# Kernel optimization log

Measured on AMD Instinct MI355X. Metric: run time of the kernel, lower is better.

Reference implementation:

```python
import jax, jax.numpy as jnp
import numpy as np


def setup_inputs() -> dict:
    key = jax.random.key(0)
    ks = jax.random.split(key, 7)
    B, S, D_IN, D_K, D_V = 4, 4096, 1024, 64, 64
    s = 1.0 / np.sqrt(D_IN)
    return {
        "query": jax.random.normal(ks[0], (B, S, D_IN), jnp.float32),
        "key": jax.random.normal(ks[1], (B, S, D_IN), jnp.float32),
        "value": jax.random.normal(ks[2], (B, S, D_IN), jnp.float32),
        "Wq": jax.random.normal(ks[3], (D_IN, D_K), jnp.float32) * s,
        "bq": jnp.zeros((D_K,), jnp.float32),
        "Wk": jax.random.normal(ks[4], (D_IN, D_K), jnp.float32) * s,
        "bk": jnp.zeros((D_K,), jnp.float32),
        "Wv": jax.random.normal(ks[5], (D_IN, D_V), jnp.float32) * s,
        "bv": jnp.zeros((D_V,), jnp.float32),
    }


def reference(query, key, value, Wq, bq, Wk, bk, Wv, bv):
    # q(query) is computed twice in the original but is identical; compute once.
    q = query @ Wq + bq            # [B,S,dk]
    k = key @ Wk + bk              # [B,S,dk]
    v = value @ Wv + bv            # [B,S,dv]
    scale = jnp.asarray(q.shape[-1] ** 0.5, q.dtype)
    scores = jnp.einsum("bqd,bkd->bqk", q, k) / scale  # [B,S,S]
    probs = jax.nn.softmax(scores, axis=-1)
    return jnp.einsum("bqk,bkd->bqd", probs, v)        # [B,S,dv]
```

## Files before the change

### kernel.cpp

```cpp
#include <hip/hip_runtime.h>
#include <cmath>

constexpr int B_  = 4;
constexpr int S_  = 4096;
constexpr int DIN = 1024;
constexpr int DH  = 64;

typedef short bf16x8 __attribute__((ext_vector_type(8)));
typedef float f32x4  __attribute__((ext_vector_type(4)));

#define GPTR(p) (const __attribute__((address_space(1))) unsigned int*)(p)
#define LPTR(p) (__attribute__((address_space(3))) unsigned int*)(p)

__device__ __forceinline__ ushort f2bf(float x) {
    unsigned int u = __float_as_uint(x);
    return (ushort)((u + 0x7FFFu + ((u >> 16) & 1u)) >> 16);
}

__device__ __forceinline__ bf16x8 cvt8(f32x4 a, f32x4 b) {
    union { bf16x8 v; ushort u[8]; } r;
    r.u[0] = f2bf(a[0]); r.u[1] = f2bf(a[1]); r.u[2] = f2bf(a[2]); r.u[3] = f2bf(a[3]);
    r.u[4] = f2bf(b[0]); r.u[5] = f2bf(b[1]); r.u[6] = f2bf(b[2]); r.u[7] = f2bf(b[3]);
    return r.v;
}

#define QSCALE 0.18033688011112042f

__global__ __launch_bounds__(256) void setup_w(
    const float* __restrict__ Wq, const float* __restrict__ Wk,
    const float* __restrict__ Wv, ushort* __restrict__ Wt_g)
{
    const int y = blockIdx.y;
    const float* W = (y == 0) ? Wq : (y == 1) ? Wk : Wv;
    const int g    = blockIdx.x * 256 + threadIdx.x;
    const int lane = g & 63;
    const int nt   = (g >> 6) & 3;
    const int ks   = (g >> 8) & 1;
    const int it   = g >> 9;
    const int m    = lane & 15;
    const int quad = lane >> 4;
    const int n    = nt * 16 + m;
    const int k0   = it * 64 + (ks * 4 + quad) * 8;
    union { uint4 q; ushort u[8]; } r;
    #pragma unroll
    for (int i = 0; i < 8; ++i) r.u[i] = f2bf(W[(size_t)(k0 + i) * DH + n]);
    *(uint4*)(Wt_g + ((size_t)y << 16) + (size_t)g * 8) = r.q;
}

__global__ __launch_bounds__(256, 4) void proj_kernel(
    const float* __restrict__ Xq, const float* __restrict__ Xk, const float* __restrict__ Xv,
    const float* __restrict__ bq, const float* __restrict__ bk, const float* __restrict__ bv,
    const ushort* __restrict__ Wt_g,
    ushort* __restrict__ Qb, ushort* __restrict__ Kb, ushort* __restrict__ Vt)
{
    __shared__ __align__(16) ushort xlds[16384];

    const int y = blockIdx.y;
    const float *X, *bias;
    if (y == 0)      { X = Xq; bias = bq; }
    else if (y == 1) { X = Xk; bias = bk; }
    else             { X = Xv; bias = bv; }

    const int tid  = threadIdx.x;
    const int w    = tid >> 6;
    const int lane = tid & 63;
    const int m    = lane & 15;
    const int quad = lane >> 4;
    const int row0 = blockIdx.x * 16;

    {
        f32x4 va[8], vb[8];
        #pragma unroll
        for (int r = 0; r < 4; ++r) {
            const float* src = X + (size_t)(row0 + w * 4 + r) * DIN + lane * 8;
            #pragma unroll
            for (int sg = 0; sg < 2; ++sg) {
                va[r * 2 + sg] = *(const f32x4*)(src + sg * 512);
                vb[r * 2 + sg] = *(const f32x4*)(src + sg * 512 + 4);
            }
        }
        __builtin_amdgcn_sched_barrier(0);
        #pragma unroll
        for (int r = 0; r < 4; ++r) {
            const int row = w * 4 + r;
            #pragma unroll
            for (int sg = 0; sg < 2; ++sg) {
                const int wi = sg * 8 + (lane >> 3);
                const int fx = (lane & 7) ^ (row & 7);
                *(bf16x8*)&xlds[((wi * 16 + row) * 8 + fx) * 8] =
                    cvt8(va[r * 2 + sg], vb[r * 2 + sg]);
            }
        }
    }
    __syncthreads();

    const float bias_v = bias[w * 16 + m];
    const ushort* wbase = Wt_g + ((size_t)y << 16) + (size_t)(w * 64 + lane) * 8;

    f32x4 acc = {};
    bf16x8 wf0 = *(const bf16x8*)(wbase);
    bf16x8 wf1 = *(const bf16x8*)(wbase + 2048);
    #pragma unroll
    for (int wi = 0; wi < 16; ++wi) {
        bf16x8 nf0 = wf0, nf1 = wf1;
        if (wi < 15) {
            nf0 = *(const bf16x8*)(wbase + (size_t)(wi + 1) * 4096);
            nf1 = *(const bf16x8*)(wbase + (size_t)(wi + 1) * 4096 + 2048);
        }
        const bf16x8 a0 = *(const bf16x8*)&xlds[((wi * 16 + m) * 8 + ( quad      ^ (m & 7))) * 8];
        const bf16x8 a1 = *(const bf16x8*)&xlds[((wi * 16 + m) * 8 + ((4 + quad) ^ (m & 7))) * 8];
        acc = __builtin_amdgcn_mfma_f32_16x16x32_bf16(a0, wf0, acc, 0, 0, 0);
        acc = __builtin_amdgcn_mfma_f32_16x16x32_bf16(a1, wf1, acc, 0, 0, 0);
        wf0 = nf0; wf1 = nf1;
    }

    if (y < 2) {
        ushort* Out = (y == 0) ? Qb : Kb;
        const float sc = (y == 0) ? QSCALE : 1.0f;
        #pragma unroll
        for (int j = 0; j < 4; ++j) {
            const int row = row0 + quad * 4 + j;
            Out[(size_t)row * DH + w * 16 + m] = f2bf((acc[j] + bias_v) * sc);
        }
    } else {
        __syncthreads();
        ushort (*Vx)[32] = (ushort(*)[32])xlds;
        #pragma unroll
        for (int j = 0; j < 4; ++j)
            Vx[w * 16 + m][quad * 4 + j] = f2bf(acc[j] + bias_v);
        __syncthreads();
        const int batch = row0 >> 12;
        const int s0    = row0 & 4095;
        if (tid < 128) {
            const int d = tid >> 1, h = tid & 1;
            const uint4 v = *(const uint4*)&Vx[d][h * 8];
            *(uint4*)(Vt + ((size_t)batch * 64 + d) * S_ + s0 + h * 8) = v;
        }
    }
}

__global__ __launch_bounds__(512, 4) void attn_kernel(
    const ushort* __restrict__ Qb, const ushort* __restrict__ Kb,
    const ushort* __restrict__ Vt, float* __restrict__ Opart, float* __restrict__ Lpart)
{
    __shared__ ushort Ks[2][4096];
    __shared__ ushort Vs[2][4096];
    __shared__ ushort Pt[128 * 72];

    const int tid  = threadIdx.x;
    const int w    = tid >> 6;
    const int lane = tid & 63;
    const int m    = lane & 15;
    const int quad = lane >> 4;

    const int u  = blockIdx.x;
    const int c  = (u & 7) * 2 + ((u >> 3) >> 5);
    const int qt = (u >> 3) & 31;
    const int b  = c >> 2, jc = c & 3;
    const int q0 = qt * 128;

    bf16x8 qf[2];
    #pragma unroll
    for (int ks = 0; ks < 2; ++ks)
        qf[ks] = *(const bf16x8*)(Qb + (size_t)(b * S_ + q0 + w * 16 + m) * 64
                                     + ks * 32 + quad * 8);
    asm volatile("s_waitcnt vmcnt(0)" ::: "memory");
    __builtin_amdgcn_sched_barrier(0);

    f32x4 acc_o[4] = {};
    float Lp[4] = {};

    const ushort* kbase = Kb + (size_t)b * S_ * 64;
    const ushort* vbase = Vt + (size_t)b * 64 * S_;

    auto stage = [&](int jt, int buf) {
        const int slot = w * 64 + lane;
        const int j = slot >> 3, cc = slot & 7;
        __builtin_amdgcn_global_load_lds(
            GPTR(kbase + (size_t)(jt * 64 + j) * 64 + ((cc ^ (j & 7)) * 8)),
            LPTR(&Ks[buf][slot * 8]), 16, 0, 0);
        __builtin_amdgcn_global_load_lds(
            GPTR(vbase + (size_t)j * S_ + jt * 64 + ((cc ^ (j & 7)) * 8)),
            LPTR(&Vs[buf][slot * 8]), 16, 0, 0);
    };

    stage(jc * 16 + 0, 0);
    stage(jc * 16 + 1, 1);

    for (int it = 0; it < 16; ++it) {
        if (it < 15) asm volatile("s_waitcnt vmcnt(2)" ::: "memory");
        else         asm volatile("s_waitcnt vmcnt(0)" ::: "memory");
        __builtin_amdgcn_sched_barrier(0);
        __builtin_amdgcn_s_barrier();
        __builtin_amdgcn_sched_barrier(0);

        const ushort* ksb = Ks[it & 1];
        const ushort* vsb = Vs[it & 1];

        f32x4 acc_s[4] = {};
        #pragma unroll
        for (int ks = 0; ks < 2; ++ks)
            #pragma unroll
            for (int jt4 = 0; jt4 < 4; ++jt4) {
                const int j = jt4 * 16 + m;
                const bf16x8 kf = *(const bf16x8*)&ksb[j * 64 + (((ks * 4 + quad) ^ (j & 7)) * 8)];
                acc_s[jt4] = __builtin_amdgcn_mfma_f32_16x16x32_bf16(
                    qf[ks], kf, acc_s[jt4], 0, 0, 0);
            }

        #pragma unroll
        for (int jt4 = 0; jt4 < 4; ++jt4)
            #pragma unroll
            for (int r = 0; r < 4; ++r) {
                const float e = exp2f(acc_s[jt4][r]);
                Lp[r] += e;
                Pt[(w * 16 + quad * 4 + r) * 72 + jt4 * 16 + m] = f2bf(e);
            }

        #pragma unroll
        for (int jc2 = 0; jc2 < 2; ++jc2) {
            const bf16x8 pf = *(const bf16x8*)&Pt[(w * 16 + m) * 72 + jc2 * 32 + quad * 8];
            #pragma unroll
            for (int dt = 0; dt < 4; ++dt) {
                const int d = dt * 16 + m;
                const bf16x8 vf = *(const bf16x8*)&vsb[d * 64 + (((jc2 * 4 + quad) ^ (d & 7)) * 8)];
                acc_o[dt] = __builtin_amdgcn_mfma_f32_16x16x32_bf16(pf, vf, acc_o[dt], 0, 0, 0);
            }
        }

        __builtin_amdgcn_sched_barrier(0);
        __builtin_amdgcn_s_barrier();
        __builtin_amdgcn_sched_barrier(0);
        if (it + 2 < 16) stage(jc * 16 + it + 2, it & 1);
    }

    #pragma unroll
    for (int r = 0; r < 4; ++r) {
        float s = Lp[r];
        #pragma unroll
        for (int off = 1; off < 16; off <<= 1)
            s += __shfl_xor(s, off, 64);
        Lp[r] = s;
    }

    const size_t bj = (size_t)(b * 4 + jc);
    float* Ob = Opart + (bj << 18);
    #pragma unroll
    for (int dt = 0; dt < 4; ++dt)
        #pragma unroll
        for (int r = 0; r < 4; ++r) {
            const int row = q0 + w * 16 + quad * 4 + r;
            Ob[(size_t)row * 64 + dt * 16 + m] = acc_o[dt][r];
        }
    if (m == 0) {
        #pragma unroll
        for (int r = 0; r < 4; ++r)
            Lpart[bj * 4096 + q0 + w * 16 + quad * 4 + r] = Lp[r];
    }
}

__global__ __launch_bounds__(256) void reduce_kernel(
    const float* __restrict__ Opart, const float* __restrict__ Lpart, float* __restrict__ out)
{
    const int g    = blockIdx.x * 256 + threadIdx.x;
    const int base = g << 2;
    const int b    = base >> 18;
    const int rem  = base & 0x3FFFF;
    const int q    = rem >> 6;
    float4 o = make_float4(0.f, 0.f, 0.f, 0.f);
    float  l = 0.f;
    #pragma unroll
    for (int jcc = 0; jcc < 4; ++jcc) {
        const float4 p = *(const float4*)(Opart + (((size_t)(b * 4 + jcc)) << 18) + rem);
        o.x += p.x; o.y += p.y; o.z += p.z; o.w += p.w;
        l += Lpart[(size_t)(b * 4 + jcc) * 4096 + q];
    }
    const float inv = 1.0f / l;
    o.x *= inv; o.y *= inv; o.z *= inv; o.w *= inv;
    *(float4*)(out + base) = o;
}

extern "C" void kernel_launch(void* const* d_in, const int* in_sizes, int n_in,
                              void* d_out, int out_size, void* d_ws, size_t ws_size,
                              hipStream_t stream)
{
    const float* query = (const float*)d_in[0];
    const float* key_  = (const float*)d_in[1];
    const float* value = (const float*)d_in[2];
    const float* Wq    = (const float*)d_in[3];
    const float* bq    = (const float*)d_in[4];
    const float* Wk    = (const float*)d_in[5];
    const float* bk    = (const float*)d_in[6];
    const float* Wv    = (const float*)d_in[7];
    const float* bv    = (const float*)d_in[8];
    float* out = (float*)d_out;

    char* ws = (char*)d_ws;
    ushort* Qb    = (ushort*)(ws);
    ushort* Kb    = (ushort*)(ws + (2  << 20));
    ushort* Vt    = (ushort*)(ws + (4  << 20));
    float*  Opart = (float*) (ws + (6  << 20));
    float*  Lpart = (float*) (ws + (22 << 20));
    ushort* Wt_g  = (ushort*)(ws + (6  << 20));

    setup_w<<<dim3(32, 3), 256, 0, stream>>>(Wq, Wk, Wv, Wt_g);
    proj_kernel<<<dim3(1024, 3), 256, 0, stream>>>(
        query, key_, value, bq, bk, bv, Wt_g, Qb, Kb, Vt);
    attn_kernel<<<dim3(512), 512, 0, stream>>>(Qb, Kb, Vt, Opart, Lpart);
    reduce_kernel<<<dim3(1024), 256, 0, stream>>>(Opart, Lpart, out);
}
```

Baseline: 249.8 us.

## Fuse split-KV reduction into attention kernel via last-block atomic counter

```diff
diff --git a/kernel.cpp b/kernel.cpp
--- a/kernel.cpp
+++ b/kernel.cpp
@@ -28,9 +28,10 @@
 
 __global__ __launch_bounds__(256) void setup_w(
     const float* __restrict__ Wq, const float* __restrict__ Wk,
-    const float* __restrict__ Wv, ushort* __restrict__ Wt_g)
+    const float* __restrict__ Wv, ushort* __restrict__ Wt_g, int* __restrict__ cnt)
 {
     const int y = blockIdx.y;
+    if (y == 0 && blockIdx.x == 0 && threadIdx.x < 128) cnt[threadIdx.x] = 0;
     const float* W = (y == 0) ? Wq : (y == 1) ? Wk : Wv;
     const int g    = blockIdx.x * 256 + threadIdx.x;
     const int lane = g & 63;
@@ -141,11 +142,13 @@
 
 __global__ __launch_bounds__(512, 4) void attn_kernel(
     const ushort* __restrict__ Qb, const ushort* __restrict__ Kb,
-    const ushort* __restrict__ Vt, float* __restrict__ Opart, float* __restrict__ Lpart)
+    const ushort* __restrict__ Vt, float* __restrict__ Opart,
+    float* __restrict__ Lpart, int* __restrict__ cnt, float* __restrict__ out)
 {
     __shared__ ushort Ks[2][4096];
     __shared__ ushort Vs[2][4096];
     __shared__ ushort Pt[128 * 72];
+    __shared__ int sOld;
 
     const int tid  = threadIdx.x;
     const int w    = tid >> 6;
@@ -257,27 +260,32 @@
         for (int r = 0; r < 4; ++r)
             Lpart[bj * 4096 + q0 + w * 16 + quad * 4 + r] = Lp[r];
     }
-}
-
-__global__ __launch_bounds__(256) void reduce_kernel(
-    const float* __restrict__ Opart, const float* __restrict__ Lpart, float* __restrict__ out)
-{
-    const int g    = blockIdx.x * 256 + threadIdx.x;
-    const int base = g << 2;
-    const int b    = base >> 18;
-    const int rem  = base & 0x3FFFF;
-    const int q    = rem >> 6;
-    float4 o = make_float4(0.f, 0.f, 0.f, 0.f);
-    float  l = 0.f;
-    #pragma unroll
-    for (int jcc = 0; jcc < 4; ++jcc) {
-        const float4 p = *(const float4*)(Opart + (((size_t)(b * 4 + jcc)) << 18) + rem);
-        o.x += p.x; o.y += p.y; o.z += p.z; o.w += p.w;
-        l += Lpart[(size_t)(b * 4 + jcc) * 4096 + q];
-    }
-    const float inv = 1.0f / l;
-    o.x *= inv; o.y *= inv; o.z *= inv; o.w *= inv;
-    *(float4*)(out + base) = o;
+
+    __threadfence();
+    __syncthreads();
+    if (tid == 0) sOld = atomicAdd(&cnt[b * 32 + qt], 1);
+    __syncthreads();
+    if (sOld == 3) {
+        __threadfence();
+        float* Of = out + ((size_t)b * S_ + q0) * DH;
+        for (int i = tid; i < 128 * 16; i += 512) {
+            const int r    = i >> 4;
+            const int col4 = (i & 15) * 4;
+            float4 o = make_float4(0.f, 0.f, 0.f, 0.f);
+            float  l = 0.f;
+            #pragma unroll
+            for (int jcc = 0; jcc < 4; ++jcc) {
+                const float4 p = *(const float4*)(
+                    Opart + (((size_t)(b * 4 + jcc)) << 18) + (size_t)(q0 + r) * 64 + col4);
+                o.x += p.x; o.y += p.y; o.z += p.z; o.w += p.w;
+                l += Lpart[(size_t)(b * 4 + jcc) * 4096 + q0 + r];
+            }
+            const float inv = 1.0f / l;
+            o.x *= inv; o.y *= inv; o.z *= inv; o.w *= inv;
+            *(float4*)(Of + (size_t)r * 64 + col4) = o;
+        }
+        if (tid == 0) cnt[b * 32 + qt] = 0;
+    }
 }
 
 extern "C" void kernel_launch(void* const* d_in, const int* in_sizes, int n_in,
@@ -301,11 +309,11 @@
     ushort* Vt    = (ushort*)(ws + (4  << 20));
     float*  Opart = (float*) (ws + (6  << 20));
     float*  Lpart = (float*) (ws + (22 << 20));
+    int*    cnt   = (int*)   (ws + (22 << 20) + (1 << 18));
     ushort* Wt_g  = (ushort*)(ws + (6  << 20));
 
-    setup_w<<<dim3(32, 3), 256, 0, stream>>>(Wq, Wk, Wv, Wt_g);
+    setup_w<<<dim3(32, 3), 256, 0, stream>>>(Wq, Wk, Wv, Wt_g, cnt);
     proj_kernel<<<dim3(1024, 3), 256, 0, stream>>>(
         query, key_, value, bq, bk, bv, Wt_g, Qb, Kb, Vt);
-    attn_kernel<<<dim3(512), 512, 0, stream>>>(Qb, Kb, Vt, Opart, Lpart);
-    reduce_kernel<<<dim3(1024), 256, 0, stream>>>(Opart, Lpart, out);
-}
+    attn_kernel<<<dim3(512), 512, 0, stream>>>(Qb, Kb, Vt, Opart, Lpart, cnt, out);
+}
```

Result: slower. 395.0 us (+58.1%).
